# Optimization experiments

Hardware: AMD Instinct MI355X
Metric: run time of the kernel (lower is better)

## Reference

```python
import jax, jax.numpy as jnp
import numpy as np

L = 5      # n_levels
NH = 4     # num_heads
P = 4      # num_points
E = 256    # embed_dims
C = 256    # bev_dims
HB = 128
WB = 128
NQ = HB * WB
HD = E // NH
NL = 6     # num_layers
FF = 2 * E # ffn hidden


def setup_inputs() -> dict:
    key = jax.random.key(0)
    ks = jax.random.split(key, 12)
    s = 0.02
    def n(k, shape):
        return jax.random.normal(k, shape, jnp.float32) * s
    return dict(
        feat_bev=jax.random.normal(ks[0], (L, 1, C, HB, WB), jnp.float32),
        norm0_g=jnp.ones((L, C), jnp.float32), norm0_b=jnp.zeros((L, C), jnp.float32),
        in_w=n(ks[1], (C * L, E)), in_b=jnp.zeros((E,), jnp.float32),
        pos_row=n(ks[2], (HB, E // 2)), pos_col=n(ks[3], (WB, E // 2)),
        off_w=n(ks[4], (NL, E, NH * L * P * 2)), off_b=n(ks[5], (NL, NH * L * P * 2)),
        aw_w=n(ks[6], (NL, E, NH * L * P)), aw_b=jnp.zeros((NL, NH * L * P), jnp.float32),
        val_w=n(ks[7], (NL, C, E)), val_b=jnp.zeros((NL, E), jnp.float32),
        out_w=n(ks[8], (NL, E, E)), out_b=jnp.zeros((NL, E), jnp.float32),
        ln1_g=jnp.ones((NL, E), jnp.float32), ln1_b=jnp.zeros((NL, E), jnp.float32),
        ln2_g=jnp.ones((NL, E), jnp.float32), ln2_b=jnp.zeros((NL, E), jnp.float32),
        ffn_w1=n(ks[9], (NL, E, FF)), ffn_b1=jnp.zeros((NL, FF), jnp.float32),
        ffn_w2=n(ks[10], (NL, FF, E)), ffn_b2=jnp.zeros((NL, E), jnp.float32),
    )


def _ln(x, g, b):
    m = x.mean(-1, keepdims=True)
    v = ((x - m) ** 2).mean(-1, keepdims=True)
    return (x - m) * jax.lax.rsqrt(v + 1e-5) * g + b


def reference(feat_bev, norm0_g, norm0_b, in_w, in_b, pos_row, pos_col,
              off_w, off_b, aw_w, aw_b, val_w, val_b, out_w, out_b,
              ln1_g, ln1_b, ln2_g, ln2_b, ffn_w1, ffn_b1, ffn_w2, ffn_b2):
    Lv, bs, Cc, H, W = feat_bev.shape
    nq = H * W
    # per-level LN over channels (norm_layer0)
    f = feat_bev.transpose(0, 1, 3, 4, 2).reshape(Lv, bs, nq, Cc)
    f = _ln(f, norm0_g[:, None, None, :], norm0_b[:, None, None, :])  # [L, bs, nq, C]
    # input_proj on channel-concat of levels (level-major block rows of in_w)
    q = jnp.einsum('lbnc,lce->bne', f, in_w.reshape(Lv, Cc, E)) + in_b  # [bs, nq, E]
    # learned positional encoding: pos[h, w] = cat(col[w], row[h])
    pos = jnp.concatenate([
        jnp.broadcast_to(pos_col[None, :, :], (H, W, E // 2)),
        jnp.broadcast_to(pos_row[:, None, :], (H, W, E // 2))], -1).reshape(1, nq, E)
    # reference points (pixel centers, normalized)
    ys, xs = jnp.meshgrid(jnp.arange(H, dtype=jnp.float32) + 0.5,
                          jnp.arange(W, dtype=jnp.float32) + 0.5, indexing='ij')
    ref = jnp.stack([xs.ravel() / W, ys.ravel() / H], -1)  # [nq, 2] (x, y)
    norm = jnp.array([W, H], jnp.float32)
    b_ix = jnp.arange(bs)[:, None, None, None, None]
    h_ix = jnp.arange(NH)[None, None, :, None, None]
    l_ix = jnp.arange(Lv)[None, None, None, :, None]
    for i in range(NL):
        qp = q + pos
        off = (qp @ off_w[i] + off_b[i]).reshape(bs, nq, NH, Lv, P, 2)
        aw = jax.nn.softmax((qp @ aw_w[i] + aw_b[i]).reshape(bs, nq, NH, Lv * P), -1)
        aw = aw.reshape(bs, nq, NH, Lv, P)
        loc = ref[None, :, None, None, None, :] + off / norm
        x = loc[..., 0] * W - 0.5
        y = loc[..., 1] * H - 0.5
        x0 = jnp.floor(x); y0 = jnp.floor(y)
        fx = x - x0; fy = y - y0
        x0i = x0.astype(jnp.int32); y0i = y0.astype(jnp.int32)
        # per-layer value projection of normed multi-level features
        val = (jnp.einsum('lbnc,ce->blne', f, val_w[i]) + val_b[i]).reshape(bs, Lv, nq, NH, HD)
        acc = jnp.zeros((bs, nq, NH, HD), q.dtype)
        for dx, dy, wgt in ((0, 0, (1 - fx) * (1 - fy)), (1, 0, fx * (1 - fy)),
                            (0, 1, (1 - fx) * fy), (1, 1, fx * fy)):
            ix = x0i + dx; iy = y0i + dy
            valid = ((ix >= 0) & (ix < W) & (iy >= 0) & (iy < H)).astype(q.dtype)
            sidx = jnp.clip(iy, 0, H - 1) * W + jnp.clip(ix, 0, W - 1)
            g = val[b_ix, l_ix, sidx, h_ix]  # [bs, nq, NH, Lv, P, HD]
            acc = acc + jnp.einsum('bqhlp,bqhlpd->bqhd', wgt * valid * aw, g)
        q = q + (acc.reshape(bs, nq, NH * HD) @ out_w[i] + out_b[i])
        q = _ln(q, ln1_g[i], ln1_b[i])
        q = q + jax.nn.relu(q @ ffn_w1[i] + ffn_b1[i]) @ ffn_w2[i] + ffn_b2[i]
        q = _ln(q, ln2_g[i], ln2_b[i])
    return q.transpose(0, 2, 1).reshape(bs, E, H, W)
```

## Files before the change

kernel.cpp:

```cpp
#include <hip/hip_runtime.h>
#include <hip/hip_bf16.h>
#include <stdint.h>

static constexpr int kL  = 5;
static constexpr int kNH = 4;
static constexpr int kP  = 4;
static constexpr int kE  = 256;
static constexpr int kC  = 256;
static constexpr int kH  = 128;
static constexpr int kW  = 128;
static constexpr int kNQ = kH * kW;
static constexpr int kNL = 6;
static constexpr int kFF = 2 * kE;
static constexpr int kCOMB = 240;

typedef short bf16x8 __attribute__((ext_vector_type(8)));
typedef float f32x4 __attribute__((ext_vector_type(4)));

__device__ __forceinline__ short f2bf(float x) {
  union { float f; uint32_t u; } v; v.f = x;
  uint32_t r = v.u + 0x7fffu + ((v.u >> 16) & 1u);
  return (short)(r >> 16);
}
__device__ __forceinline__ uint32_t pack2(float a, float b) {
  return (uint32_t)(unsigned short)f2bf(a) | ((uint32_t)(unsigned short)f2bf(b) << 16);
}
__device__ __forceinline__ float bflo(uint32_t u) { return __uint_as_float(u << 16); }
__device__ __forceinline__ float bfhi(uint32_t u) { return __uint_as_float(u & 0xffff0000u); }
__device__ __forceinline__ float bf2f(unsigned short u) {
  return __uint_as_float((uint32_t)u << 16);
}

__device__ __forceinline__ void gl_lds16(const void* g, void* l) {
  __builtin_amdgcn_global_load_lds(
      (const __attribute__((address_space(1))) void*)g,
      (__attribute__((address_space(3))) void*)l, 16, 0, 0);
}

template <int BM, int MODE, int RB>
__global__ __launch_bounds__(512, MODE == 0 ? 4 : 2) void gemm2_kernel(
    const short* __restrict__ A, long sAb, int lda,
    const short* __restrict__ BT, int ldbt, int Kb, int nbatch,
    const float* __restrict__ bias,
    float* Cf, short* __restrict__ Cb, int ldc, int relu, long zouts,
    const void* resid, const float* __restrict__ lng,
    const float* __restrict__ lnb, short* __restrict__ qp,
    const float* __restrict__ pos_row, const float* __restrict__ pos_col,
    const short* __restrict__ w2BT, const float* __restrict__ w2B,
    short* __restrict__ out2) {
  static_assert(BM == 64, "layout assumes BM=64");
  constexpr bool FUSED = (MODE == 3 || MODE == 4 || MODE == 5);
  constexpr int BK = 64;
  constexpr int KG = 2;
  constexpr int NW = 8;
  constexpr int MT = 2;
  constexpr int NT = 4;
  constexpr int AG = (BM / 16) * KG;
  constexpr int BG = 16 * KG;
  constexpr int ASZ = BM * BK;
  constexpr int BSZ = 256 * BK;
  __shared__ short smem[2 * ASZ + 2 * BSZ + (FUSED ? 64 * 280 : 0)];
  short* const Asm = smem;
  short* const Bsm = smem + 2 * ASZ;
  short* const qpS = smem + 2 * ASZ + 2 * BSZ;
  float2(*const lnpart)[4] = (float2(*)[4])smem;
  const int tid = threadIdx.x;
  const int wave = tid >> 6, lane = tid & 63;
  const int wy = wave >> 2, wx = wave & 3;
  const long row0 = (long)blockIdx.y * BM;
  const int col0 = blockIdx.x * 256;
  const int srow = lane >> 2;
  const int skof = ((lane & 3) ^ (srow & 3)) * 8;
  const int fr = lane & 15, fq = lane >> 4;
  const int ua = (fr * 4 + (fq ^ (fr & 3))) * 8;
  f32x4 acc[MT][NT] = {};
  const int KT = Kb >> 6;
  const int NTILES = nbatch * KT;

  auto stage_tile = [&](int buf, int bb, int kt) {
    const short* Ab = A + (long)bb * sAb + row0 * lda;
    const short* Bb = BT + (long)col0 * ldbt + (long)bb * Kb;
    int k0 = kt * BK;
#pragma unroll
    for (int t = wave; t < AG + BG; t += NW) {
      if (t < AG) {
        int rg = t >> 1, kg = t & 1;
        gl_lds16(Ab + (long)(rg * 16 + srow) * lda + k0 + kg * 32 + skof,
                 &Asm[buf * ASZ + t * 512]);
      } else {
        int u = t - AG;
        int rg = u >> 1, kg = u & 1;
        gl_lds16(Bb + (long)(rg * 16 + srow) * ldbt + k0 + kg * 32 + skof,
                 &Bsm[buf * BSZ + u * 512]);
      }
    }
  };

  int cur = 0;
  stage_tile(0, 0, 0);
  __syncthreads();
  int sb = 0, sk = 0;
  for (int idx = 0; idx < NTILES; ++idx) {
    if (idx + 1 < NTILES) {
      if (++sk == KT) { sk = 0; ++sb; }
      stage_tile(cur ^ 1, sb, sk);
    }
#pragma unroll
    for (int kk = 0; kk < KG; ++kk) {
      bf16x8 af[MT], bfv[NT];
#pragma unroll
      for (int t = 0; t < MT; ++t)
        af[t] = *(const bf16x8*)&Asm[cur * ASZ + ((wy * MT + t) * KG + kk) * 512 + ua];
#pragma unroll
      for (int t = 0; t < NT; ++t)
        bfv[t] = *(const bf16x8*)&Bsm[cur * BSZ + ((wx * 4 + t) * KG + kk) * 512 + ua];
#pragma unroll
      for (int mt = 0; mt < MT; ++mt)
#pragma unroll
        for (int nt = 0; nt < NT; ++nt)
          acc[mt][nt] = __builtin_amdgcn_mfma_f32_16x16x32_bf16(
              af[mt], bfv[nt], acc[mt][nt], 0, 0, 0);
    }
    __syncthreads();
    cur ^= 1;
  }

  const int colb = col0 + wx * 64 + fr;
  const long rowb = row0 + wy * 32 + fq * 4;

  if (MODE == 0) {
    const long zoff = (long)blockIdx.x * zouts;
#pragma unroll
    for (int mt = 0; mt < MT; ++mt)
#pragma unroll
      for (int rr = 0; rr < 4; ++rr) {
        long row = rowb + mt * 16 + rr;
#pragma unroll
        for (int nt = 0; nt < NT; ++nt) {
          int col = colb + nt * 16;
          float v = acc[mt][nt][rr] + bias[col];
          if (relu) v = fmaxf(v, 0.f);
          if (Cf) Cf[row * ldc + col] = v;
          if (Cb) Cb[zoff + row * ldc + col] = f2bf(v);
        }
      }
  } else if (MODE == 5) {
#pragma unroll
    for (int mt = 0; mt < MT; ++mt)
#pragma unroll
      for (int rr = 0; rr < 4; ++rr) {
        long row = rowb + mt * 16 + rr;
        int rl = wy * 32 + mt * 16 + fq * 4 + rr;
        int wpos = (int)row & (kW - 1), hpos = (int)row >> 7;
#pragma unroll
        for (int nt = 0; nt < NT; ++nt) {
          int col = colb + nt * 16;
          float v = acc[mt][nt][rr] + bias[col];
          Cf[row * 256 + col] = v;
          float pv = (col < 128) ? pos_col[wpos * 128 + col]
                                 : pos_row[hpos * 128 + (col - 128)];
          qpS[rl * 280 + col] = f2bf(v + pv);
        }
      }
  } else {
    const float* residf = (const float*)resid;
    const unsigned short* residb = (const unsigned short*)resid;
#pragma unroll
    for (int mt = 0; mt < MT; ++mt)
#pragma unroll
      for (int rr = 0; rr < 4; ++rr) {
        long row = rowb + mt * 16 + rr;
        float s = 0.f, s2 = 0.f;
#pragma unroll
        for (int nt = 0; nt < NT; ++nt) {
          int col = colb + nt * 16;
          float rv = RB ? bf2f(residb[row * 256 + col])
                        : residf[row * 256 + col];
          float v = acc[mt][nt][rr] + bias[col] + rv;
          acc[mt][nt][rr] = v;
          s += v; s2 += v * v;
        }
#pragma unroll
        for (int o = 8; o > 0; o >>= 1) {
          s += __shfl_xor(s, o);
          s2 += __shfl_xor(s2, o);
        }
        if (fr == 0) {
          int rl = wy * 32 + mt * 16 + fq * 4 + rr;
          lnpart[rl][wx] = make_float2(s, s2);
        }
      }
    __syncthreads();
#pragma unroll
    for (int mt = 0; mt < MT; ++mt)
#pragma unroll
      for (int rr = 0; rr < 4; ++rr) {
        int rl = wy * 32 + mt * 16 + fq * 4 + rr;
        long row = rowb + mt * 16 + rr;
        float s = 0.f, s2 = 0.f;
#pragma unroll
        for (int c = 0; c < 4; ++c) {
          s += lnpart[rl][c].x; s2 += lnpart[rl][c].y;
        }
        float m = s * (1.f / 256);
        float var = s2 * (1.f / 256) - m * m;
        float rs = rsqrtf(var + 1e-5f);
        int wpos = (int)row & (kW - 1), hpos = (int)row >> 7;
#pragma unroll
        for (int nt = 0; nt < NT; ++nt) {
          int col = colb + nt * 16;
          float y = (acc[mt][nt][rr] - m) * rs * lng[col] + lnb[col];
          if (Cf) Cf[row * 256 + col] = y;
          if (MODE != 3 && Cb) Cb[row * 256 + col] = f2bf(y);
          if (MODE == 1 && qp) {
            float pv = (col < 128) ? pos_col[wpos * 128 + col]
                                   : pos_row[hpos * 128 + (col - 128)];
            qp[row * 256 + col] = f2bf(y + pv);
          }
          if (MODE == 3) {
            float pv = (col < 128) ? pos_col[wpos * 128 + col]
                                   : pos_row[hpos * 128 + (col - 128)];
            qpS[rl * 280 + col] = f2bf(y + pv);
          }
          if (MODE == 4) qpS[rl * 280 + col] = f2bf(y);
        }
      }
  }
  if constexpr (FUSED) {
    __syncthreads();
    constexpr int ld2 = (MODE == 4) ? 512 : 256;
    constexpr int MT2 = BM / 16;
    constexpr int NT2 = (MODE == 4) ? 8 : 4;
    auto stageW = [&](int buf, int t2) {
      int hf = t2 >> 2;
      int k0 = (t2 & 3) * BK;
#pragma unroll
      for (int u = wave; u < BG; u += NW) {
        int rg = u >> 1, kg = u & 1;
        gl_lds16(w2BT + (long)(hf * 256 + rg * 16 + srow) * 256 + k0 +
                     kg * 32 + skof,
                 &Bsm[buf * BSZ + u * 512]);
      }
    };
    f32x4 acc2[MT2][NT] = {};
    stageW(cur, 0);
    __syncthreads();
    for (int t2 = 0; t2 < NT2; ++t2) {
      if (t2 + 1 < NT2) stageW(cur ^ 1, t2 + 1);
      int k0 = (t2 & 3) * BK;
#pragma unroll
      for (int kk = 0; kk < KG; ++kk) {
        bf16x8 av[MT2], bv[NT];
#pragma unroll
        for (int mt = 0; mt < MT2; ++mt)
          av[mt] = *(const bf16x8*)&qpS[(mt * 16 + fr) * 280 + k0 +
                                        kk * 32 + fq * 8];
#pragma unroll
        for (int t = 0; t < NT; ++t)
          bv[t] = *(const bf16x8*)&Bsm[cur * BSZ + ((wx * 4 + t) * KG + kk) *
                                           512 + ua];
#pragma unroll
        for (int mt = 0; mt < MT2; ++mt)
#pragma unroll
          for (int t = 0; t < NT; ++t)
            acc2[mt][t] = __builtin_amdgcn_mfma_f32_16x16x32_bf16(
                av[mt], bv[t], acc2[mt][t], 0, 0, 0);
      }
      if ((t2 & 3) == 3) {
        int hf = t2 >> 2;
#pragma unroll
        for (int mt = 0; mt < MT2; ++mt)
#pragma unroll
          for (int rr = 0; rr < 4; ++rr) {
            long row = row0 + mt * 16 + fq * 4 + rr;
#pragma unroll
            for (int nt = 0; nt < NT; ++nt) {
              int oc = hf * 256 + wx * 64 + nt * 16 + fr;
              float v = acc2[mt][nt][rr] + w2B[oc];
              if (MODE == 4) v = fmaxf(v, 0.f);
              out2[row * ld2 + oc] = f2bf(v);
            }
          }
#pragma unroll
        for (int mt = 0; mt < MT2; ++mt)
#pragma unroll
          for (int t = 0; t < NT; ++t)
            acc2[mt][t] = f32x4{0.f, 0.f, 0.f, 0.f};
      }
      __syncthreads();
      cur ^= 1;
    }
  }
}

__global__ __launch_bounds__(256) void convert_all_kernel(
    const float* __restrict__ in_w, const float* __restrict__ val_w,
    const float* __restrict__ out_w, const float* __restrict__ ffn_w1,
    const float* __restrict__ ffn_w2, const float* __restrict__ off_w,
    const float* __restrict__ aw_w, const float* __restrict__ off_b,
    const float* __restrict__ aw_b,
    short* __restrict__ inT, short* __restrict__ valT, short* __restrict__ outT,
    short* __restrict__ ffn1T, short* __restrict__ ffn2T,
    short* __restrict__ combT, float* __restrict__ comb_bias) {
  long e = (long)blockIdx.x * 256 + threadIdx.x;
  if (e < 327680) {
    int idx = (int)e;
    int n = idx / 1280, k = idx - n * 1280;
    inT[idx] = f2bf(in_w[(long)k * 256 + n]);
    return;
  }
  e -= 327680;
  if (e < 393216) {
    int z = (int)(e >> 16), idx = (int)e & 65535;
    int n = idx >> 8, k = idx & 255;
    valT[e] = f2bf(val_w[((long)z * 256 + k) * 256 + n]);
    return;
  }
  e -= 393216;
  if (e < 393216) {
    int z = (int)(e >> 16), idx = (int)e & 65535;
    int n = idx >> 8, k = idx & 255;
    outT[e] = f2bf(out_w[((long)z * 256 + k) * 256 + n]);
    return;
  }
  e -= 393216;
  if (e < 786432) {
    int z = (int)(e / 131072);
    int idx = (int)(e - (long)z * 131072);
    int n = idx >> 8, k = idx & 255;
    ffn1T[e] = f2bf(ffn_w1[((long)z * 256 + k) * 512 + n]);
    return;
  }
  e -= 786432;
  if (e < 786432) {
    int z = (int)(e / 131072);
    int idx = (int)(e - (long)z * 131072);
    int n = idx >> 9, k = idx & 511;
    ffn2T[e] = f2bf(ffn_w2[((long)z * 512 + k) * 256 + n]);
    return;
  }
  e -= 786432;
  {
    int z = (int)(e >> 16), idx = (int)e & 65535;
    int n = idx >> 8, k = idx & 255;
    float v = 0.f;
    if (n < 160) v = off_w[((long)z * 256 + k) * 160 + n];
    else if (n < kCOMB) v = aw_w[((long)z * 256 + k) * 80 + (n - 160)];
    combT[e] = f2bf(v);
    if (k == 0)
      comb_bias[z * 256 + n] =
          (n < 160) ? off_b[z * 160 + n]
                    : (n < kCOMB ? aw_b[z * 80 + (n - 160)] : 0.f);
  }
}

__global__ __launch_bounds__(256) void ln_fused_kernel(
    const float* __restrict__ feat, const float* __restrict__ g,
    const float* __restrict__ b, short* __restrict__ f) {
  __shared__ float tile[256][33];
  __shared__ float2 part[8][32];
  __shared__ float mS[32], rsS[32];
  int l = blockIdx.y;
  int n0 = blockIdx.x * 32;
  int tx = threadIdx.x & 31;
  int ty = threadIdx.x >> 5;
  float s = 0.f, s2 = 0.f;
#pragma unroll 8
  for (int j = 0; j < 32; ++j) {
    int c = ty * 32 + j;
    float v = feat[((long)(l * kC + c)) * kNQ + n0 + tx];
    tile[c][tx] = v;
    s += v; s2 += v * v;
  }
  part[ty][tx] = make_float2(s, s2);
  __syncthreads();
  if (ty == 0) {
    float ss = 0.f, ss2 = 0.f;
#pragma unroll
    for (int j = 0; j < 8; ++j) {
      ss += part[j][tx].x; ss2 += part[j][tx].y;
    }
    float m = ss * (1.f / kC);
    float var = ss2 * (1.f / kC) - m * m;
    mS[tx] = m;
    rsS[tx] = rsqrtf(var + 1e-5f);
  }
  __syncthreads();
  int c = threadIdx.x;
  float gv = g[l * kC + c], bv = b[l * kC + c];
#pragma unroll 8
  for (int r = 0; r < 32; ++r) {
    float v = (tile[c][r] - mS[r]) * rsS[r] * gv + bv;
    f[((long)l * kNQ + n0 + r) * kC + c] = f2bf(v);
  }
}

__global__ __launch_bounds__(256) void sample_kernel(
    const unsigned short* __restrict__ comb, const short* __restrict__ val,
    short* __restrict__ accb) {
  __shared__ float2 ic[4][2][4][85];
  int wv = threadIdx.x >> 6;
  int lane = threadIdx.x & 63;
  int half = lane >> 5;
  int hl = lane & 31;
  int n = blockIdx.x * 8 + wv * 2 + half;
  int wq = n & (kW - 1);
  int hq = n >> 7;
  const unsigned short* cb = comb + (long)n * 256;
#pragma unroll
  for (int h = 0; h < 4; ++h) {
    float raw = (hl < 20) ? bf2f(cb[160 + h * 20 + hl]) : -1e30f;
    float mx = raw;
#pragma unroll
    for (int o = 16; o > 0; o >>= 1) mx = fmaxf(mx, __shfl_xor(mx, o));
    float ev = (hl < 20) ? __expf(raw - mx) : 0.f;
    float se = ev;
#pragma unroll
    for (int o = 16; o > 0; o >>= 1) se += __shfl_xor(se, o);
    if (hl < 20) {
      float awv = ev / se;
      int l = hl >> 2;
      float ox = bf2f(cb[h * 40 + hl * 2 + 0]);
      float oy = bf2f(cb[h * 40 + hl * 2 + 1]);
      float x = (float)wq + ox;
      float y = (float)hq + oy;
      float x0f = floorf(x), y0f = floorf(y);
      float fx = x - x0f, fy = y - y0f;
      int x0 = (int)x0f, y0 = (int)y0f;
#pragma unroll
      for (int c = 0; c < 4; ++c) {
        int dx = c & 1, dy = c >> 1;
        int ix = x0 + dx, iy = y0 + dy;
        float wgt = (dx ? fx : 1.f - fx) * (dy ? fy : 1.f - fy);
        bool valid = (ix >= 0 && ix < kW && iy >= 0 && iy < kH);
        int cix = min(max(ix, 0), kW - 1);
        int ciy = min(max(iy, 0), kH - 1);
        int sidx = ciy * kW + cix;
        int byteoff = (l * kNQ + sidx) * (kE * 2);
        float coef = valid ? awv * wgt : 0.f;
        ic[wv][half][h][hl * 4 + c] = make_float2(__int_as_float(byteoff), coef);
      }
    }
  }
  __syncthreads();
  int h2 = (lane >> 3) & 3;
  int ch8 = (lane & 7) * 8;
  const char* vb = (const char*)val + (h2 * 64 + ch8) * 2;
  const float2* icp = &ic[wv][half][h2][0];
  float a0 = 0.f, a1 = 0.f, a2 = 0.f, a3 = 0.f;
  float a4 = 0.f, a5 = 0.f, a6 = 0.f, a7 = 0.f;
#pragma unroll 4
  for (int j = 0; j < 80; ++j) {
    float2 oc = icp[j];
    int off = __float_as_int(oc.x);
    uint4 u = *(const uint4*)(vb + off);
    float cf = oc.y;
    a0 += cf * bflo(u.x); a1 += cf * bfhi(u.x);
    a2 += cf * bflo(u.y); a3 += cf * bfhi(u.y);
    a4 += cf * bflo(u.z); a5 += cf * bfhi(u.z);
    a6 += cf * bflo(u.w); a7 += cf * bfhi(u.w);
  }
  uint4 o;
  o.x = pack2(a0, a1); o.y = pack2(a2, a3);
  o.z = pack2(a4, a5); o.w = pack2(a6, a7);
  *(uint4*)(accb + (long)n * kE + h2 * 64 + ch8) = o;
}

__global__ __launch_bounds__(256) void transpose_kernel(
    const float* __restrict__ q, float* __restrict__ out) {
  __shared__ float t[32][33];
  int eb = blockIdx.x * 32, nb = blockIdx.y * 32;
  int tx = threadIdx.x & 31, ty = threadIdx.x >> 5;
#pragma unroll
  for (int j = 0; j < 4; ++j)
    t[ty + j * 8][tx] = q[(long)(nb + ty + j * 8) * kE + eb + tx];
  __syncthreads();
#pragma unroll
  for (int j = 0; j < 4; ++j)
    out[(long)(eb + ty + j * 8) * kNQ + nb + tx] = t[tx][ty + j * 8];
}

extern "C" void kernel_launch(void* const* d_in, const int* in_sizes, int n_in,
                              void* d_out, int out_size, void* d_ws,
                              size_t ws_size, hipStream_t stream) {
  const float* feat    = (const float*)d_in[0];
  const float* norm0_g = (const float*)d_in[1];
  const float* norm0_b = (const float*)d_in[2];
  const float* in_w    = (const float*)d_in[3];
  const float* in_b    = (const float*)d_in[4];
  const float* pos_row = (const float*)d_in[5];
  const float* pos_col = (const float*)d_in[6];
  const float* off_w   = (const float*)d_in[7];
  const float* off_b   = (const float*)d_in[8];
  const float* aw_w    = (const float*)d_in[9];
  const float* aw_b    = (const float*)d_in[10];
  const float* val_w   = (const float*)d_in[11];
  const float* val_b   = (const float*)d_in[12];
  const float* out_w   = (const float*)d_in[13];
  const float* out_b   = (const float*)d_in[14];
  const float* ln1_g   = (const float*)d_in[15];
  const float* ln1_b   = (const float*)d_in[16];
  const float* ln2_g   = (const float*)d_in[17];
  const float* ln2_b   = (const float*)d_in[18];
  const float* ffn_w1  = (const float*)d_in[19];
  const float* ffn_b1  = (const float*)d_in[20];
  const float* ffn_w2  = (const float*)d_in[21];
  const float* ffn_b2  = (const float*)d_in[22];

  char* p = (char*)d_ws;
  auto alloc = [&](size_t bytes) -> char* {
    char* r = p;
    p += (bytes + 255) & ~(size_t)255;
    return r;
  };
  const size_t valSlab = (size_t)kL * kNQ * kE;
  short* f_bf    = (short*)alloc((size_t)kL * kNQ * kC * 2);
  short* val_bf  = (short*)alloc(3 * valSlab * 2);
  float* q       = (float*)alloc((size_t)kNQ * kE * 4);
  short* qbf     = (short*)alloc((size_t)kNQ * kE * 2);
  short* accb    = (short*)alloc((size_t)kNQ * kE * 2);
  short* hid_bf  = (short*)alloc((size_t)kNQ * kFF * 2);
  short* comb_bf = (short*)alloc((size_t)kNQ * 256 * 2);
  float* comb_b  = (float*)alloc((size_t)kNL * 256 * 4);
  short* inT     = (short*)alloc((size_t)256 * 1280 * 2);
  short* valT    = (short*)alloc((size_t)kNL * 256 * 256 * 2);
  short* outT    = (short*)alloc((size_t)kNL * 256 * 256 * 2);
  short* ffn1T   = (short*)alloc((size_t)kNL * 512 * 256 * 2);
  short* ffn2T   = (short*)alloc((size_t)kNL * 256 * 512 * 2);
  short* combT   = (short*)alloc((size_t)kNL * 256 * 256 * 2);

  convert_all_kernel<<<12032, 256, 0, stream>>>(
      in_w, val_w, out_w, ffn_w1, ffn_w2, off_w, aw_w, off_b, aw_b,
      inT, valT, outT, ffn1T, ffn2T, combT, comb_b);

  ln_fused_kernel<<<dim3(kNQ / 32, kL), 256, 0, stream>>>(feat, norm0_g,
                                                          norm0_b, f_bf);

  const long zouts = (long)kL * kNQ * 256 - 256;
  gemm2_kernel<64, 0, 0><<<dim3(3, kL * kNQ / 64), 512, 0, stream>>>(
      f_bf, 0, kC, valT, 256, 256, 1, val_b,
      nullptr, val_bf, kE, 0, zouts, nullptr, nullptr, nullptr, nullptr,
      nullptr, nullptr, nullptr, nullptr, nullptr);

  gemm2_kernel<64, 5, 0><<<dim3(1, kNQ / 64), 512, 0, stream>>>(
      f_bf, (long)kNQ * kC, kC, inT, 1280, 256, kL, in_b,
      q, nullptr, 256, 0, 0, nullptr, nullptr, nullptr, nullptr,
      pos_row, pos_col, combT, comb_b, comb_bf);

  for (int i = 0; i < kNL; ++i) {
    const short* outT_i  = outT + (long)i * 256 * 256;
    const short* f1T_i   = ffn1T + (long)i * 512 * 256;
    const short* f2T_i   = ffn2T + (long)i * 256 * 512;

    sample_kernel<<<kNQ / 8, 256, 0, stream>>>(
        (const unsigned short*)comb_bf, val_bf + (long)(i % 3) * valSlab,
        accb);
    if (i == 2) {
      gemm2_kernel<64, 0, 0><<<dim3(3, kL * kNQ / 64), 512, 0, stream>>>(
          f_bf, 0, kC, valT + 3 * 256 * 256, 256, 256, 1, val_b + 3 * kE,
          nullptr, val_bf, kE, 0, zouts, nullptr, nullptr, nullptr, nullptr,
          nullptr, nullptr, nullptr, nullptr, nullptr);
    }
    gemm2_kernel<64, 4, 0><<<dim3(1, kNQ / 64), 512, 0, stream>>>(
        accb, 0, kE, outT_i, 256, 256, 1, out_b + (long)i * kE,
        nullptr, qbf, 256, 0, 0, q, ln1_g + (long)i * kE, ln1_b + (long)i * kE,
        nullptr, nullptr, nullptr, f1T_i, ffn_b1 + (long)i * kFF, hid_bf);
    if (i + 1 < kNL) {
      gemm2_kernel<64, 3, 1><<<dim3(1, kNQ / 64), 512, 0, stream>>>(
          hid_bf, 0, kFF, f2T_i, 512, 512, 1, ffn_b2 + (long)i * kE,
          q, nullptr, 256, 0, 0, qbf, ln2_g + (long)i * kE,
          ln2_b + (long)i * kE, nullptr, pos_row, pos_col,
          combT + (long)(i + 1) * 256 * 256, comb_b + (i + 1) * 256, comb_bf);
    } else {
      gemm2_kernel<64, 1, 1><<<dim3(1, kNQ / 64), 512, 0, stream>>>(
          hid_bf, 0, kFF, f2T_i, 512, 512, 1, ffn_b2 + (long)i * kE,
          q, nullptr, 256, 0, 0, qbf, ln2_g + (long)i * kE,
          ln2_b + (long)i * kE, nullptr, nullptr, nullptr,
          nullptr, nullptr, nullptr);
    }
  }

  transpose_kernel<<<dim3(kE / 32, kNQ / 32), 256, 0, stream>>>(q,
                                                                (float*)d_out);
}
```

Before: 959.1 us.

## Fuse per-layer out-proj, LN1, FFN, LN2 and combined projection into one kernel

Two per-layer GEMM launches (out-proj+LN1+FFN1 and FFN2+LN2+offset/weight projection) become a single layer_kernel that handles one 64-row block through all stages. The LN1 output stays in shared memory as the FFN2 residual, so the bf16 qbf round trip through global memory and one launch per layer go away. hid_bf still goes through global memory. The cost is a longer kernel with more registers, which may lower occupancy, and a residual now read from bf16 shared memory, as before.

```diff
diff --git a/kernel.cpp b/kernel.cpp
--- a/kernel.cpp
+++ b/kernel.cpp
@@ -43,13 +43,11 @@
     const short* __restrict__ BT, int ldbt, int Kb, int nbatch,
     const float* __restrict__ bias,
     float* Cf, short* __restrict__ Cb, int ldc, int relu, long zouts,
-    const void* resid, const float* __restrict__ lng,
-    const float* __restrict__ lnb, short* __restrict__ qp,
     const float* __restrict__ pos_row, const float* __restrict__ pos_col,
     const short* __restrict__ w2BT, const float* __restrict__ w2B,
     short* __restrict__ out2) {
   static_assert(BM == 64, "layout assumes BM=64");
-  constexpr bool FUSED = (MODE == 3 || MODE == 4 || MODE == 5);
+  constexpr bool FUSED = (MODE == 5);
   constexpr int BK = 64;
   constexpr int KG = 2;
   constexpr int NW = 8;
@@ -63,7 +61,6 @@
   short* const Asm = smem;
   short* const Bsm = smem + 2 * ASZ;
   short* const qpS = smem + 2 * ASZ + 2 * BSZ;
-  float2(*const lnpart)[4] = (float2(*)[4])smem;
   const int tid = threadIdx.x;
   const int wave = tid >> 6, lane = tid & 63;
   const int wy = wave >> 2, wx = wave & 3;
@@ -162,21 +159,151 @@
           qpS[rl * 280 + col] = f2bf(v + pv);
         }
       }
-  } else {
-    const float* residf = (const float*)resid;
-    const unsigned short* residb = (const unsigned short*)resid;
+  }
+  if constexpr (FUSED) {
+    auto stageW = [&](int buf, int t2) {
+      int k0 = (t2 & 3) * BK;
+#pragma unroll
+      for (int u = wave; u < BG; u += NW) {
+        int rg = u >> 1, kg = u & 1;
+        gl_lds16(w2BT + (long)(rg * 16 + srow) * 256 + k0 + kg * 32 + skof,
+                 &Bsm[buf * BSZ + u * 512]);
+      }
+    };
+    f32x4 acc2[4][NT] = {};
+    stageW(cur, 0);
+    __syncthreads();
+    for (int t2 = 0; t2 < 4; ++t2) {
+      if (t2 + 1 < 4) stageW(cur ^ 1, t2 + 1);
+      int k0 = t2 * BK;
+#pragma unroll
+      for (int kk = 0; kk < KG; ++kk) {
+        bf16x8 av[4], bv[NT];
+#pragma unroll
+        for (int mt = 0; mt < 4; ++mt)
+          av[mt] = *(const bf16x8*)&qpS[(mt * 16 + fr) * 280 + k0 +
+                                        kk * 32 + fq * 8];
+#pragma unroll
+        for (int t = 0; t < NT; ++t)
+          bv[t] = *(const bf16x8*)&Bsm[cur * BSZ + ((wx * 4 + t) * KG + kk) *
+                                           512 + ua];
+#pragma unroll
+        for (int mt = 0; mt < 4; ++mt)
+#pragma unroll
+          for (int t = 0; t < NT; ++t)
+            acc2[mt][t] = __builtin_amdgcn_mfma_f32_16x16x32_bf16(
+                av[mt], bv[t], acc2[mt][t], 0, 0, 0);
+      }
+      __syncthreads();
+      cur ^= 1;
+    }
+#pragma unroll
+    for (int mt = 0; mt < 4; ++mt)
+#pragma unroll
+      for (int rr = 0; rr < 4; ++rr) {
+        long row = row0 + mt * 16 + fq * 4 + rr;
+#pragma unroll
+        for (int nt = 0; nt < NT; ++nt) {
+          int oc = wx * 64 + nt * 16 + fr;
+          out2[row * 256 + oc] = f2bf(acc2[mt][nt][rr] + w2B[oc]);
+        }
+      }
+  }
+}
+
+template <int LAST>
+__global__ __launch_bounds__(512, 2) void layer_kernel(
+    const short* __restrict__ accb, const short* __restrict__ outTW,
+    const float* __restrict__ outb, float* __restrict__ q,
+    const float* __restrict__ ln1g, const float* __restrict__ ln1b,
+    const short* __restrict__ f1T, const float* __restrict__ f1b,
+    short* __restrict__ hid, const short* __restrict__ f2T,
+    const float* __restrict__ f2b, const float* __restrict__ ln2g,
+    const float* __restrict__ ln2b, const float* __restrict__ pos_row,
+    const float* __restrict__ pos_col, const short* __restrict__ combTW,
+    const float* __restrict__ comb_b, short* __restrict__ comb_bf) {
+  constexpr int BK = 64, KG = 2, NW = 8, MT = 2, NT = 4;
+  constexpr int AG = 8, BG = 32;
+  constexpr int ASZ = 64 * BK, BSZ = 256 * BK;
+  __shared__ short smem[2 * ASZ + 2 * BSZ + 64 * 280];
+  short* const Asm = smem;
+  short* const Bsm = smem + 2 * ASZ;
+  short* const qpS = smem + 2 * ASZ + 2 * BSZ;
+  float2* const lnpart = (float2*)Asm;
+  const int tid = threadIdx.x;
+  const int wave = tid >> 6, lane = tid & 63;
+  const int wy = wave >> 2, wx = wave & 3;
+  const long row0 = (long)blockIdx.y * 64;
+  const int srow = lane >> 2;
+  const int skof = ((lane & 3) ^ (srow & 3)) * 8;
+  const int fr = lane & 15, fq = lane >> 4;
+  const int ua = (fr * 4 + (fq ^ (fr & 3))) * 8;
+  const int colb = wx * 64 + fr;
+  const long rowb = row0 + wy * 32 + fq * 4;
+  f32x4 acc[MT][NT];
+
+  auto run_gemm = [&](const short* Ab, int lda, const short* Bb, int ldbt,
+                      int ntiles) {
+#pragma unroll
+    for (int mt = 0; mt < MT; ++mt)
+#pragma unroll
+      for (int nt = 0; nt < NT; ++nt) acc[mt][nt] = f32x4{0.f, 0.f, 0.f, 0.f};
+    auto stage = [&](int buf, int kt) {
+      int k0 = kt * BK;
+#pragma unroll
+      for (int t = wave; t < AG + BG; t += NW) {
+        if (t < AG) {
+          int rg = t >> 1, kg = t & 1;
+          gl_lds16(Ab + (long)(rg * 16 + srow) * lda + k0 + kg * 32 + skof,
+                   &Asm[buf * ASZ + t * 512]);
+        } else {
+          int u = t - AG, rg = u >> 1, kg = u & 1;
+          gl_lds16(Bb + (long)(rg * 16 + srow) * ldbt + k0 + kg * 32 + skof,
+                   &Bsm[buf * BSZ + u * 512]);
+        }
+      }
+    };
+    stage(0, 0);
+    __syncthreads();
+    int cur = 0;
+    for (int t = 0; t < ntiles; ++t) {
+      if (t + 1 < ntiles) stage(cur ^ 1, t + 1);
+#pragma unroll
+      for (int kk = 0; kk < KG; ++kk) {
+        bf16x8 af[MT], bfv[NT];
+#pragma unroll
+        for (int i = 0; i < MT; ++i)
+          af[i] = *(const bf16x8*)&Asm[cur * ASZ +
+                                       ((wy * MT + i) * KG + kk) * 512 + ua];
+#pragma unroll
+        for (int i = 0; i < NT; ++i)
+          bfv[i] = *(const bf16x8*)&Bsm[cur * BSZ +
+                                        ((wx * 4 + i) * KG + kk) * 512 + ua];
+#pragma unroll
+        for (int mt = 0; mt < MT; ++mt)
+#pragma unroll
+          for (int nt = 0; nt < NT; ++nt)
+            acc[mt][nt] = __builtin_amdgcn_mfma_f32_16x16x32_bf16(
+                af[mt], bfv[nt], acc[mt][nt], 0, 0, 0);
+      }
+      __syncthreads();
+      cur ^= 1;
+    }
+  };
+
+  auto ln_epilogue = [&](const float* bias, auto residf, const float* g,
+                         const float* b, auto writer) {
 #pragma unroll
     for (int mt = 0; mt < MT; ++mt)
 #pragma unroll
       for (int rr = 0; rr < 4; ++rr) {
         long row = rowb + mt * 16 + rr;
+        int rl = wy * 32 + mt * 16 + fq * 4 + rr;
         float s = 0.f, s2 = 0.f;
 #pragma unroll
         for (int nt = 0; nt < NT; ++nt) {
           int col = colb + nt * 16;
-          float rv = RB ? bf2f(residb[row * 256 + col])
-                        : residf[row * 256 + col];
-          float v = acc[mt][nt][rr] + bias[col] + rv;
+          float v = acc[mt][nt][rr] + bias[col] + residf(row, col, rl);
           acc[mt][nt][rr] = v;
           s += v; s2 += v * v;
         }
@@ -185,10 +312,7 @@
           s += __shfl_xor(s, o);
           s2 += __shfl_xor(s2, o);
         }
-        if (fr == 0) {
-          int rl = wy * 32 + mt * 16 + fq * 4 + rr;
-          lnpart[rl][wx] = make_float2(s, s2);
-        }
+        if (fr == 0) lnpart[rl * 4 + wx] = make_float2(s, s2);
       }
     __syncthreads();
 #pragma unroll
@@ -200,67 +324,58 @@
         float s = 0.f, s2 = 0.f;
 #pragma unroll
         for (int c = 0; c < 4; ++c) {
-          s += lnpart[rl][c].x; s2 += lnpart[rl][c].y;
+          s += lnpart[rl * 4 + c].x;
+          s2 += lnpart[rl * 4 + c].y;
         }
         float m = s * (1.f / 256);
         float var = s2 * (1.f / 256) - m * m;
         float rs = rsqrtf(var + 1e-5f);
-        int wpos = (int)row & (kW - 1), hpos = (int)row >> 7;
 #pragma unroll
         for (int nt = 0; nt < NT; ++nt) {
           int col = colb + nt * 16;
-          float y = (acc[mt][nt][rr] - m) * rs * lng[col] + lnb[col];
-          if (Cf) Cf[row * 256 + col] = y;
-          if (MODE != 3 && Cb) Cb[row * 256 + col] = f2bf(y);
-          if (MODE == 1 && qp) {
-            float pv = (col < 128) ? pos_col[wpos * 128 + col]
-                                   : pos_row[hpos * 128 + (col - 128)];
-            qp[row * 256 + col] = f2bf(y + pv);
-          }
-          if (MODE == 3) {
-            float pv = (col < 128) ? pos_col[wpos * 128 + col]
-                                   : pos_row[hpos * 128 + (col - 128)];
-            qpS[rl * 280 + col] = f2bf(y + pv);
-          }
-          if (MODE == 4) qpS[rl * 280 + col] = f2bf(y);
-        }
-      }
-  }
-  if constexpr (FUSED) {
-    __syncthreads();
-    constexpr int ld2 = (MODE == 4) ? 512 : 256;
-    constexpr int MT2 = BM / 16;
-    constexpr int NT2 = (MODE == 4) ? 8 : 4;
+          float y = (acc[mt][nt][rr] - m) * rs * g[col] + b[col];
+          writer(rl, row, col, y);
+        }
+      }
+  };
+
+  auto run_gemm2 = [&](const short* WT, int nhalf, int ld2, bool dorelu,
+                       const float* b2, short* out2) {
     auto stageW = [&](int buf, int t2) {
-      int hf = t2 >> 2;
-      int k0 = (t2 & 3) * BK;
+      int hf = t2 >> 2, k0 = (t2 & 3) * BK;
 #pragma unroll
       for (int u = wave; u < BG; u += NW) {
         int rg = u >> 1, kg = u & 1;
-        gl_lds16(w2BT + (long)(hf * 256 + rg * 16 + srow) * 256 + k0 +
-                     kg * 32 + skof,
+        gl_lds16(WT + (long)(hf * 256 + rg * 16 + srow) * 256 + k0 + kg * 32 +
+                     skof,
                  &Bsm[buf * BSZ + u * 512]);
       }
     };
-    f32x4 acc2[MT2][NT] = {};
-    stageW(cur, 0);
+    const int NT2 = nhalf * 4;
+    f32x4 acc2[4][NT];
+#pragma unroll
+    for (int mt = 0; mt < 4; ++mt)
+#pragma unroll
+      for (int t = 0; t < NT; ++t) acc2[mt][t] = f32x4{0.f, 0.f, 0.f, 0.f};
+    stageW(0, 0);
     __syncthreads();
+    int cur = 0;
     for (int t2 = 0; t2 < NT2; ++t2) {
       if (t2 + 1 < NT2) stageW(cur ^ 1, t2 + 1);
       int k0 = (t2 & 3) * BK;
 #pragma unroll
       for (int kk = 0; kk < KG; ++kk) {
-        bf16x8 av[MT2], bv[NT];
-#pragma unroll
-        for (int mt = 0; mt < MT2; ++mt)
-          av[mt] = *(const bf16x8*)&qpS[(mt * 16 + fr) * 280 + k0 +
-                                        kk * 32 + fq * 8];
+        bf16x8 av[4], bv[NT];
+#pragma unroll
+        for (int mt = 0; mt < 4; ++mt)
+          av[mt] = *(const bf16x8*)&qpS[(mt * 16 + fr) * 280 + k0 + kk * 32 +
+                                        fq * 8];
 #pragma unroll
         for (int t = 0; t < NT; ++t)
-          bv[t] = *(const bf16x8*)&Bsm[cur * BSZ + ((wx * 4 + t) * KG + kk) *
-                                           512 + ua];
-#pragma unroll
-        for (int mt = 0; mt < MT2; ++mt)
+          bv[t] = *(const bf16x8*)&Bsm[cur * BSZ +
+                                       ((wx * 4 + t) * KG + kk) * 512 + ua];
+#pragma unroll
+        for (int mt = 0; mt < 4; ++mt)
 #pragma unroll
           for (int t = 0; t < NT; ++t)
             acc2[mt][t] = __builtin_amdgcn_mfma_f32_16x16x32_bf16(
@@ -269,28 +384,51 @@
       if ((t2 & 3) == 3) {
         int hf = t2 >> 2;
 #pragma unroll
-        for (int mt = 0; mt < MT2; ++mt)
+        for (int mt = 0; mt < 4; ++mt)
 #pragma unroll
           for (int rr = 0; rr < 4; ++rr) {
             long row = row0 + mt * 16 + fq * 4 + rr;
 #pragma unroll
             for (int nt = 0; nt < NT; ++nt) {
               int oc = hf * 256 + wx * 64 + nt * 16 + fr;
-              float v = acc2[mt][nt][rr] + w2B[oc];
-              if (MODE == 4) v = fmaxf(v, 0.f);
+              float v = acc2[mt][nt][rr] + b2[oc];
+              if (dorelu) v = fmaxf(v, 0.f);
               out2[row * ld2 + oc] = f2bf(v);
             }
           }
 #pragma unroll
-        for (int mt = 0; mt < MT2; ++mt)
-#pragma unroll
-          for (int t = 0; t < NT; ++t)
-            acc2[mt][t] = f32x4{0.f, 0.f, 0.f, 0.f};
+        for (int mt = 0; mt < 4; ++mt)
+#pragma unroll
+          for (int t = 0; t < NT; ++t) acc2[mt][t] = f32x4{0.f, 0.f, 0.f, 0.f};
       }
       __syncthreads();
       cur ^= 1;
     }
-  }
+  };
+
+  run_gemm(accb + row0 * 256, 256, outTW, 256, 4);
+  ln_epilogue(
+      outb, [&](long row, int col, int) { return q[row * 256 + col]; }, ln1g,
+      ln1b,
+      [&](int rl, long row, int col, float y) { qpS[rl * 280 + col] = f2bf(y); });
+  run_gemm2(f1T, 2, 512, true, f1b, hid);
+  run_gemm(hid + row0 * 512, 512, f2T, 512, 8);
+  ln_epilogue(
+      f2b,
+      [&](long row, int col, int rl) {
+        return bf2f((unsigned short)qpS[rl * 280 + col]);
+      },
+      ln2g, ln2b,
+      [&](int rl, long row, int col, float y) {
+        q[row * 256 + col] = y;
+        if (!LAST) {
+          int wpos = (int)row & (kW - 1), hpos = (int)row >> 7;
+          float pv = (col < 128) ? pos_col[wpos * 128 + col]
+                                 : pos_row[hpos * 128 + (col - 128)];
+          qpS[rl * 280 + col] = f2bf(y + pv);
+        }
+      });
+  if (!LAST) run_gemm2(combTW, 1, 256, false, comb_b, comb_bf);
 }
 
 __global__ __launch_bounds__(256) void convert_all_kernel(
@@ -517,7 +655,6 @@
   short* f_bf    = (short*)alloc((size_t)kL * kNQ * kC * 2);
   short* val_bf  = (short*)alloc(3 * valSlab * 2);
   float* q       = (float*)alloc((size_t)kNQ * kE * 4);
-  short* qbf     = (short*)alloc((size_t)kNQ * kE * 2);
   short* accb    = (short*)alloc((size_t)kNQ * kE * 2);
   short* hid_bf  = (short*)alloc((size_t)kNQ * kFF * 2);
   short* comb_bf = (short*)alloc((size_t)kNQ * 256 * 2);
@@ -539,13 +676,12 @@
   const long zouts = (long)kL * kNQ * 256 - 256;
   gemm2_kernel<64, 0, 0><<<dim3(3, kL * kNQ / 64), 512, 0, stream>>>(
       f_bf, 0, kC, valT, 256, 256, 1, val_b,
-      nullptr, val_bf, kE, 0, zouts, nullptr, nullptr, nullptr, nullptr,
-      nullptr, nullptr, nullptr, nullptr, nullptr);
+      nullptr, val_bf, kE, 0, zouts, nullptr, nullptr,
+      nullptr, nullptr, nullptr);
 
   gemm2_kernel<64, 5, 0><<<dim3(1, kNQ / 64), 512, 0, stream>>>(
       f_bf, (long)kNQ * kC, kC, inT, 1280, 256, kL, in_b,
-      q, nullptr, 256, 0, 0, nullptr, nullptr, nullptr, nullptr,
-      pos_row, pos_col, combT, comb_b, comb_bf);
+      q, nullptr, 256, 0, 0, pos_row, pos_col, combT, comb_b, comb_bf);
 
   for (int i = 0; i < kNL; ++i) {
     const short* outT_i  = outT + (long)i * 256 * 256;
@@ -558,25 +694,26 @@
     if (i == 2) {
       gemm2_kernel<64, 0, 0><<<dim3(3, kL * kNQ / 64), 512, 0, stream>>>(
           f_bf, 0, kC, valT + 3 * 256 * 256, 256, 256, 1, val_b + 3 * kE,
-          nullptr, val_bf, kE, 0, zouts, nullptr, nullptr, nullptr, nullptr,
-          nullptr, nullptr, nullptr, nullptr, nullptr);
-    }
-    gemm2_kernel<64, 4, 0><<<dim3(1, kNQ / 64), 512, 0, stream>>>(
-        accb, 0, kE, outT_i, 256, 256, 1, out_b + (long)i * kE,
-        nullptr, qbf, 256, 0, 0, q, ln1_g + (long)i * kE, ln1_b + (long)i * kE,
-        nullptr, nullptr, nullptr, f1T_i, ffn_b1 + (long)i * kFF, hid_bf);
+          nullptr, val_bf, kE, 0, zouts, nullptr, nullptr,
+          nullptr, nullptr, nullptr);
+    }
     if (i + 1 < kNL) {
-      gemm2_kernel<64, 3, 1><<<dim3(1, kNQ / 64), 512, 0, stream>>>(
-          hid_bf, 0, kFF, f2T_i, 512, 512, 1, ffn_b2 + (long)i * kE,
-          q, nullptr, 256, 0, 0, qbf, ln2_g + (long)i * kE,
-          ln2_b + (long)i * kE, nullptr, pos_row, pos_col,
+      layer_kernel<0><<<dim3(1, kNQ / 64), 512, 0, stream>>>(
+          accb, outT_i, out_b + (long)i * kE, q,
+          ln1_g + (long)i * kE, ln1_b + (long)i * kE,
+          f1T_i, ffn_b1 + (long)i * kFF, hid_bf,
+          f2T_i, ffn_b2 + (long)i * kE,
+          ln2_g + (long)i * kE, ln2_b + (long)i * kE,
+          pos_row, pos_col,
           combT + (long)(i + 1) * 256 * 256, comb_b + (i + 1) * 256, comb_bf);
     } else {
-      gemm2_kernel<64, 1, 1><<<dim3(1, kNQ / 64), 512, 0, stream>>>(
-          hid_bf, 0, kFF, f2T_i, 512, 512, 1, ffn_b2 + (long)i * kE,
-          q, nullptr, 256, 0, 0, qbf, ln2_g + (long)i * kE,
-          ln2_b + (long)i * kE, nullptr, nullptr, nullptr,
-          nullptr, nullptr, nullptr);
+      layer_kernel<1><<<dim3(1, kNQ / 64), 512, 0, stream>>>(
+          accb, outT_i, out_b + (long)i * kE, q,
+          ln1_g + (long)i * kE, ln1_b + (long)i * kE,
+          f1T_i, ffn_b1 + (long)i * kFF, hid_bf,
+          f2T_i, ffn_b2 + (long)i * kE,
+          ln2_g + (long)i * kE, ln2_b + (long)i * kE,
+          pos_row, pos_col, nullptr, nullptr, nullptr);
     }
   }
 
```

Result: faster. 868.3 us (-9.5%).
